# Kernel optimization log

Hardware: AMD Instinct MI355X
Metric: run time of the kernel (lower is better)

The kernel has to match this reference:

```python
import jax, jax.numpy as jnp
import numpy as np

D_MODEL = 1024
D_INNER = 2048
N_EXPERTS = 8
TOP_K = 2
INIT_STD = 0.02


def setup_inputs() -> dict:
    key = jax.random.key(0)
    ks = jax.random.split(key, 6)
    B, S = 2, 2048
    x = jax.random.normal(ks[0], (B, S, D_MODEL), dtype=jnp.float32)
    router_w = jax.random.normal(ks[1], (N_EXPERTS, D_MODEL), dtype=jnp.float32) * (INIT_STD * 0.1)
    router_b = jnp.zeros((N_EXPERTS,), dtype=jnp.float32)
    gate_w = jax.random.normal(ks[2], (N_EXPERTS, D_MODEL, D_INNER), dtype=jnp.float32) * INIT_STD
    up_w = jax.random.normal(ks[3], (N_EXPERTS, D_MODEL, D_INNER), dtype=jnp.float32) * INIT_STD
    down_w = jax.random.normal(ks[4], (N_EXPERTS, D_INNER, D_MODEL), dtype=jnp.float32) * INIT_STD
    return {"x": x, "router_w": router_w, "router_b": router_b,
            "gate_w": gate_w, "up_w": up_w, "down_w": down_w}


def reference(x, router_w, router_b, gate_w, up_w, down_w):
    # Router: softmax over experts, top-k, renormalize top-k probs.
    logits = jnp.einsum('bsd,ed->bse', x, router_w) + router_b          # [B,S,E]
    probs = jax.nn.softmax(logits, axis=-1)
    top_p, top_i = jax.lax.top_k(probs, TOP_K)                           # [B,S,K]
    top_p = top_p / jnp.sum(top_p, axis=-1, keepdims=True)
    # Per-expert combine weight: c[b,s,e] = sum_k top_p[b,s,k] * [top_i[b,s,k]==e]
    onehot = jax.nn.one_hot(top_i, N_EXPERTS, dtype=x.dtype)             # [B,S,K,E]
    combine = jnp.einsum('bsk,bske->bse', top_p, onehot)                 # [B,S,E]
    # SwiGLU FFN for every expert (dense form of the masked dispatch),
    # zeroed/weighted by combine coefficients.
    g = jnp.einsum('bsd,edf->ebsf', x, gate_w)                           # [E,B,S,F]
    u = jnp.einsum('bsd,edf->ebsf', x, up_w)
    h = jax.nn.silu(g) * u
    y = jnp.einsum('ebsf,efd->ebsd', h, down_w)                          # [E,B,S,D]
    out = jnp.einsum('ebsd,bse->bsd', y, combine)
    return out
```

## Files before the change

kernel.cpp:

```cpp
#include <hip/hip_runtime.h>
#include <hip/hip_bf16.h>
#include <stdint.h>

#define D_MODEL 1024
#define D_INNER 2048
#define NEXP 8
#define TOPK 2
#define T256 40
#define T128 72

typedef float f32x4 __attribute__((ext_vector_type(4)));
typedef short bf16x8 __attribute__((ext_vector_type(8)));

#define MEMFENCE asm volatile("" ::: "memory")

__device__ __forceinline__ unsigned short f2b(float f) {
    union { float f; uint32_t u; } v; v.f = f;
    uint32_t u = v.u;
    return (unsigned short)((u + 0x7fffu + ((u >> 16) & 1u)) >> 16);
}

__device__ __forceinline__ void gl_lds16(const void* g, void* l) {
    __builtin_amdgcn_global_load_lds((const __attribute__((address_space(1))) void*)g,
                                     (__attribute__((address_space(3))) void*)l, 16, 0, 0);
}

__global__ __launch_bounds__(256) void tcast3_kernel(
    const float* __restrict__ gw, const float* __restrict__ uw, const float* __restrict__ dw,
    unsigned short* __restrict__ gT, unsigned short* __restrict__ uT, unsigned short* __restrict__ dT)
{
    __shared__ unsigned short S[64][68];
    int which = blockIdx.z >> 3;
    int e = blockIdx.z & 7;
    const float* in; unsigned short* out; int K, N;
    if (which == 0)      { in = gw; out = gT; K = D_MODEL; N = D_INNER; }
    else if (which == 1) { in = uw; out = uT; K = D_MODEL; N = D_INNER; }
    else                 { in = dw; out = dT; K = D_INNER; N = D_MODEL; }
    int n0 = blockIdx.x * 64, k0 = blockIdx.y * 64;
    if (n0 >= N || k0 >= K) return;
    const float* ib = in + (size_t)e * K * N;
    unsigned short* ob = out + (size_t)e * N * K;
    int tid = threadIdx.x;
    int kk = tid >> 4, nn4 = (tid & 15) * 4;
#pragma unroll
    for (int j = 0; j < 4; j++) {
        int k = kk + 16 * j;
        float4 v = *(const float4*)&ib[(size_t)(k0 + k) * N + n0 + nn4];
        ushort4 s; s.x = f2b(v.x); s.y = f2b(v.y); s.z = f2b(v.z); s.w = f2b(v.w);
        *(ushort4*)&S[k][nn4] = s;
    }
    __syncthreads();
    int nn = tid >> 4, kk4 = (tid & 15) * 4;
#pragma unroll
    for (int j = 0; j < 4; j++) {
        int n = nn + 16 * j;
        ushort4 s;
        s.x = S[kk4 + 0][n]; s.y = S[kk4 + 1][n];
        s.z = S[kk4 + 2][n]; s.w = S[kk4 + 3][n];
        *(ushort4*)&ob[(size_t)(n0 + n) * K + k0 + kk4] = s;
    }
}

__global__ __launch_bounds__(64) void router_kernel(
    const float* __restrict__ x, const float* __restrict__ rw,
    const float* __restrict__ rb, unsigned short* __restrict__ xb,
    int* __restrict__ top_i, float* __restrict__ top_w, int T)
{
    int t = blockIdx.x;
    if (t >= T) return;
    int l = threadIdx.x;
    float xv[16];
#pragma unroll
    for (int i = 0; i < 16; i++) xv[i] = x[(size_t)t * D_MODEL + l + 64 * i];
#pragma unroll
    for (int i = 0; i < 16; i++) xb[(size_t)t * D_MODEL + l + 64 * i] = f2b(xv[i]);
    float logit[NEXP];
#pragma unroll
    for (int e = 0; e < NEXP; e++) {
        float acc = 0.f;
#pragma unroll
        for (int i = 0; i < 16; i++) acc += xv[i] * rw[e * D_MODEL + l + 64 * i];
#pragma unroll
        for (int s = 32; s > 0; s >>= 1) acc += __shfl_xor(acc, s, 64);
        logit[e] = acc + rb[e];
    }
    if (l == 0) {
        int i0 = 0; float m0 = logit[0];
#pragma unroll
        for (int e = 1; e < NEXP; e++) if (logit[e] > m0) { m0 = logit[e]; i0 = e; }
        int i1 = -1; float m1 = -3.0e38f;
#pragma unroll
        for (int e = 0; e < NEXP; e++) {
            if (e == i0) continue;
            if (logit[e] > m1) { m1 = logit[e]; i1 = e; }
        }
        float w0 = 1.f / (1.f + expf(m1 - m0));
        top_i[t * 2 + 0] = i0; top_i[t * 2 + 1] = i1;
        top_w[t * 2 + 0] = w0; top_w[t * 2 + 1] = 1.f - w0;
    }
}

__global__ __launch_bounds__(256) void bucket_kernel(
    const int* __restrict__ top_i, const float* __restrict__ top_w,
    int* __restrict__ meta, int* __restrict__ tok_of_slot,
    float* __restrict__ w_of_slot, int T)
{
    __shared__ int cnt[256][NEXP];
    __shared__ int pre[256][NEXP];
    __shared__ int tot[NEXP];
    __shared__ int off[NEXP + 1];
    int tid = threadIdx.x;
    int per = (T + 255) / 256;
    int t0 = tid * per;
    for (int e = 0; e < NEXP; e++) cnt[tid][e] = 0;
    for (int t = t0; t < t0 + per && t < T; t++)
        for (int k = 0; k < TOPK; k++) cnt[tid][top_i[t * 2 + k]]++;
    __syncthreads();
    if (tid < NEXP) {
        int run = 0;
        for (int i = 0; i < 256; i++) { pre[i][tid] = run; run += cnt[i][tid]; }
        tot[tid] = run;
    }
    __syncthreads();
    if (tid == 0) {
        off[0] = 0;
        for (int e = 0; e < NEXP; e++) off[e + 1] = off[e] + tot[e];
        for (int e = 0; e <= NEXP; e++) meta[e] = off[e];
        int nt = 0;
        for (int e = 0; e < NEXP; e++)
            for (int r = off[e]; r < off[e + 1]; r += 256)
                meta[16 + nt++] = (e << 16) | r;
        for (; nt < T256; nt++) meta[16 + nt] = -1;
        nt = 0;
        for (int e = 0; e < NEXP; e++)
            for (int r = off[e]; r < off[e + 1]; r += 128)
                meta[64 + nt++] = (e << 16) | r;
        for (; nt < T128; nt++) meta[64 + nt] = -1;
    }
    __syncthreads();
    int lc[NEXP];
#pragma unroll
    for (int e = 0; e < NEXP; e++) lc[e] = 0;
    for (int t = t0; t < t0 + per && t < T; t++) {
        for (int k = 0; k < TOPK; k++) {
            int e = top_i[t * 2 + k];
            int slot = off[e] + pre[tid][e] + lc[e]++;
            tok_of_slot[slot] = t;
            w_of_slot[slot] = top_w[t * 2 + k];
        }
    }
}

__global__ __launch_bounds__(512, 2) void moe_gate_up(
    const unsigned short* __restrict__ xb, const unsigned short* __restrict__ wgT,
    const unsigned short* __restrict__ wuT, const int* __restrict__ meta,
    const int* __restrict__ tok_of_slot, unsigned short* __restrict__ H)
{
    extern __shared__ __align__(16) unsigned short lds[];

    int lin = blockIdx.x;
    int strip = (lin & 7) * 2 + ((lin >> 3) & 1);
    int tix = lin >> 4;
    int packed = meta[16 + tix];
    if (packed < 0) return;
    int e = packed >> 16, row0 = packed & 0xffff;
    int Mloc = min(256, meta[e + 1] - row0);
    int f0 = strip * 128;

    int tid = threadIdx.x, wv = tid >> 6, lane = tid & 63;
    int c = tid & 7, rr = tid >> 3;

    const unsigned short* srcA[4];
    const unsigned short* srcG[2];
    const unsigned short* srcU[2];
#pragma unroll
    for (int j = 0; j < 4; j++) {
        int row = j * 64 + rr;
        int slot = row0 + ((row < Mloc) ? row : 0);
        srcA[j] = xb + (size_t)tok_of_slot[slot] * D_MODEL + 8 * (c ^ (row & 7));
    }
#pragma unroll
    for (int j = 0; j < 2; j++) {
        int row = j * 64 + rr;
        size_t wb = (size_t)e * D_MODEL * D_INNER + (size_t)(f0 + row) * D_MODEL + 8 * (c ^ (row & 7));
        srcG[j] = wgT + wb; srcU[j] = wuT + wb;
    }

    int wm = wv >> 1, wn = wv & 1;
    int lrow = lane & 15, kgrp = lane >> 4;
    int sw = lrow & 7;
    int co0 = 8 * (kgrp ^ sw);
    int co1 = 8 * ((4 + kgrp) ^ sw);

    int arow[4], brow[4];
#pragma unroll
    for (int i = 0; i < 4; i++) arow[i] = (wm * 64 + i * 16 + lrow) * 64;
#pragma unroll
    for (int i = 0; i < 4; i++) brow[i] = (wn * 64 + i * 16 + lrow) * 64;

    f32x4 accg[4][4], accu[4][4];
#pragma unroll
    for (int i = 0; i < 4; i++)
#pragma unroll
        for (int j = 0; j < 4; j++) {
            accg[i][j] = (f32x4){0.f, 0.f, 0.f, 0.f};
            accu[i][j] = (f32x4){0.f, 0.f, 0.f, 0.f};
        }

    auto stage = [&](int u) {
        int kk = u * 64;
        unsigned short* base = lds + (u & 1) * 32768;
#pragma unroll
        for (int j = 0; j < 4; j++)
            gl_lds16(srcA[j] + kk, base + (j * 512 + wv * 64) * 8);
#pragma unroll
        for (int j = 0; j < 2; j++) {
            gl_lds16(srcG[j] + kk, base + 16384 + (j * 512 + wv * 64) * 8);
            gl_lds16(srcU[j] + kk, base + 24576 + (j * 512 + wv * 64) * 8);
        }
    };

    bf16x8 a[4], bg[4], bu[4];
    auto load_frags = [&](int u, int co) {
        const unsigned short* base = lds + (u & 1) * 32768;
#pragma unroll
        for (int i = 0; i < 4; i++) a[i] = *(const bf16x8*)(base + arow[i] + co);
#pragma unroll
        for (int i = 0; i < 4; i++) bg[i] = *(const bf16x8*)(base + 16384 + brow[i] + co);
#pragma unroll
        for (int i = 0; i < 4; i++) bu[i] = *(const bf16x8*)(base + 24576 + brow[i] + co);
    };

    const int NT = D_MODEL / 64;
    stage(0);
    MEMFENCE;
    asm volatile("s_waitcnt vmcnt(0)" ::: "memory");
    __builtin_amdgcn_s_barrier();
    MEMFENCE;
    load_frags(0, co0);

    for (int t = 0; t < NT; ++t) {
        if (t + 1 < NT) stage(t + 1);
        __builtin_amdgcn_sched_barrier(0);
        __builtin_amdgcn_s_setprio(1);
#pragma unroll
        for (int fm = 0; fm < 4; fm++)
#pragma unroll
            for (int fn = 0; fn < 4; fn++) {
                accg[fm][fn] = __builtin_amdgcn_mfma_f32_16x16x32_bf16(a[fm], bg[fn], accg[fm][fn], 0, 0, 0);
                accu[fm][fn] = __builtin_amdgcn_mfma_f32_16x16x32_bf16(a[fm], bu[fn], accu[fm][fn], 0, 0, 0);
            }
        __builtin_amdgcn_s_setprio(0);
        load_frags(t, co1);
        __builtin_amdgcn_s_setprio(1);
#pragma unroll
        for (int fm = 0; fm < 4; fm++)
#pragma unroll
            for (int fn = 0; fn < 4; fn++) {
                accg[fm][fn] = __builtin_amdgcn_mfma_f32_16x16x32_bf16(a[fm], bg[fn], accg[fm][fn], 0, 0, 0);
                accu[fm][fn] = __builtin_amdgcn_mfma_f32_16x16x32_bf16(a[fm], bu[fn], accu[fm][fn], 0, 0, 0);
            }
        __builtin_amdgcn_s_setprio(0);
        __builtin_amdgcn_sched_barrier(0);
        asm volatile("s_waitcnt vmcnt(0)" ::: "memory");
        __builtin_amdgcn_s_barrier();
        MEMFENCE;
        if (t + 1 < NT) load_frags(t + 1, co0);
    }

#pragma unroll
    for (int fm = 0; fm < 4; fm++)
#pragma unroll
        for (int fn = 0; fn < 4; fn++)
#pragma unroll
            for (int r = 0; r < 4; r++) {
                int m = wm * 64 + fm * 16 + kgrp * 4 + r;
                if (m < Mloc) {
                    int n = wn * 64 + fn * 16 + lrow;
                    float g = accg[fm][fn][r], u = accu[fm][fn][r];
                    float h = g / (1.f + __expf(-g)) * u;
                    H[(size_t)(row0 + m) * D_INNER + f0 + n] = f2b(h);
                }
            }
}

__global__ __launch_bounds__(512, 2) void moe_down(
    const unsigned short* __restrict__ H, const unsigned short* __restrict__ wdT,
    const int* __restrict__ meta, const int* __restrict__ tok_of_slot,
    const float* __restrict__ w_of_slot, float* __restrict__ out, int S2)
{
    extern __shared__ __align__(16) unsigned short lds[];
    __shared__ int toks[128];
    __shared__ float wts[128];

    int lin = blockIdx.x;
    int d0 = (lin & 3) * 256;
    int tix = lin >> 2;
    int packed = meta[64 + tix];
    if (packed < 0) return;
    int e = packed >> 16, row0 = packed & 0xffff;
    int Mloc = min(128, meta[e + 1] - row0);

    int tid = threadIdx.x, wv = tid >> 6, lane = tid & 63;
    if (tid < 128) {
        bool v = tid < Mloc;
        toks[tid] = v ? tok_of_slot[row0 + tid] : 0;
        wts[tid] = v ? w_of_slot[row0 + tid] : 0.f;
    }
    int c = tid & 7, rr = tid >> 3;

    const unsigned short* srcA[2];
    const unsigned short* srcB[4];
#pragma unroll
    for (int j = 0; j < 2; j++) {
        int row = j * 64 + rr;
        int slot = min(row0 + row, S2 - 1);
        srcA[j] = H + (size_t)slot * D_INNER + 8 * (c ^ (row & 7));
    }
#pragma unroll
    for (int j = 0; j < 4; j++) {
        int row = j * 64 + rr;
        srcB[j] = wdT + (size_t)e * D_INNER * D_MODEL + (size_t)(d0 + row) * D_INNER + 8 * (c ^ (row & 7));
    }

    int wm = wv >> 2, wn = wv & 3;
    int lrow = lane & 15, kgrp = lane >> 4;
    int sw = lrow & 7;
    int co0 = 8 * (kgrp ^ sw);
    int co1 = 8 * ((4 + kgrp) ^ sw);

    int arow[4], brow[4];
#pragma unroll
    for (int i = 0; i < 4; i++) arow[i] = (wm * 64 + i * 16 + lrow) * 64;
#pragma unroll
    for (int i = 0; i < 4; i++) brow[i] = 8192 + (wn * 64 + i * 16 + lrow) * 64;

    f32x4 acc[4][4];
#pragma unroll
    for (int i = 0; i < 4; i++)
#pragma unroll
        for (int j = 0; j < 4; j++) acc[i][j] = (f32x4){0.f, 0.f, 0.f, 0.f};

    auto stage = [&](int u) {
        int kk = u * 64;
        unsigned short* base = lds + (u & 1) * 24576;
#pragma unroll
        for (int j = 0; j < 2; j++)
            gl_lds16(srcA[j] + kk, base + (j * 512 + wv * 64) * 8);
#pragma unroll
        for (int j = 0; j < 4; j++)
            gl_lds16(srcB[j] + kk, base + 8192 + (j * 512 + wv * 64) * 8);
    };

    bf16x8 a[4], b[4];
    auto load_frags = [&](int u, int co) {
        const unsigned short* base = lds + (u & 1) * 24576;
#pragma unroll
        for (int i = 0; i < 4; i++) a[i] = *(const bf16x8*)(base + arow[i] + co);
#pragma unroll
        for (int i = 0; i < 4; i++) b[i] = *(const bf16x8*)(base + brow[i] + co);
    };

    const int NT = D_INNER / 64;
    stage(0);
    MEMFENCE;
    asm volatile("s_waitcnt vmcnt(0)" ::: "memory");
    __builtin_amdgcn_s_barrier();
    MEMFENCE;
    load_frags(0, co0);

    for (int t = 0; t < NT; ++t) {
        if (t + 1 < NT) stage(t + 1);
        __builtin_amdgcn_sched_barrier(0);
        __builtin_amdgcn_s_setprio(1);
#pragma unroll
        for (int fm = 0; fm < 4; fm++)
#pragma unroll
            for (int fn = 0; fn < 4; fn++)
                acc[fm][fn] = __builtin_amdgcn_mfma_f32_16x16x32_bf16(a[fm], b[fn], acc[fm][fn], 0, 0, 0);
        __builtin_amdgcn_s_setprio(0);
        load_frags(t, co1);
        __builtin_amdgcn_s_setprio(1);
#pragma unroll
        for (int fm = 0; fm < 4; fm++)
#pragma unroll
            for (int fn = 0; fn < 4; fn++)
                acc[fm][fn] = __builtin_amdgcn_mfma_f32_16x16x32_bf16(a[fm], b[fn], acc[fm][fn], 0, 0, 0);
        __builtin_amdgcn_s_setprio(0);
        __builtin_amdgcn_sched_barrier(0);
        asm volatile("s_waitcnt vmcnt(0)" ::: "memory");
        __builtin_amdgcn_s_barrier();
        MEMFENCE;
        if (t + 1 < NT) load_frags(t + 1, co0);
    }

#pragma unroll
    for (int fm = 0; fm < 4; fm++)
#pragma unroll
        for (int fn = 0; fn < 4; fn++)
#pragma unroll
            for (int r = 0; r < 4; r++) {
                int m = wm * 64 + fm * 16 + kgrp * 4 + r;
                if (m < Mloc) {
                    int n = wn * 64 + fn * 16 + lrow;
                    atomicAdd(&out[(size_t)toks[m] * D_MODEL + d0 + n], wts[m] * acc[fm][fn][r]);
                }
            }
}

extern "C" void kernel_launch(void* const* d_in, const int* in_sizes, int n_in,
                              void* d_out, int out_size, void* d_ws, size_t ws_size,
                              hipStream_t stream) {
    const float* x  = (const float*)d_in[0];
    const float* rw = (const float*)d_in[1];
    const float* rb = (const float*)d_in[2];
    const float* gw = (const float*)d_in[3];
    const float* uw = (const float*)d_in[4];
    const float* dw = (const float*)d_in[5];
    float* out = (float*)d_out;

    int T = in_sizes[0] / D_MODEL;
    int S2 = 2 * T;

    char* ws = (char*)d_ws;
    size_t cur = 0;
    auto take = [&](size_t bytes) { char* p = ws + cur; cur = (cur + bytes + 255) & ~(size_t)255; return p; };
    int*   top_i = (int*)take((size_t)S2 * 4);
    float* top_w = (float*)take((size_t)S2 * 4);
    int*   meta  = (int*)take(1024);
    int*   tos   = (int*)take((size_t)S2 * 4);
    float* wos   = (float*)take((size_t)S2 * 4);
    unsigned short* xb  = (unsigned short*)take((size_t)T * D_MODEL * 2);
    unsigned short* wgT = (unsigned short*)take((size_t)NEXP * D_MODEL * D_INNER * 2);
    unsigned short* wuT = (unsigned short*)take((size_t)NEXP * D_MODEL * D_INNER * 2);
    unsigned short* wdT = (unsigned short*)take((size_t)NEXP * D_MODEL * D_INNER * 2);
    unsigned short* H   = (unsigned short*)take((size_t)S2 * D_INNER * 2);

    static const int GU_LDS = 2 * 32768 * 2;
    static const int DN_LDS = 2 * 24576 * 2;
    hipFuncSetAttribute((const void*)moe_gate_up,
                        hipFuncAttributeMaxDynamicSharedMemorySize, GU_LDS);
    hipFuncSetAttribute((const void*)moe_down,
                        hipFuncAttributeMaxDynamicSharedMemorySize, DN_LDS);

    hipMemsetAsync(d_out, 0, (size_t)out_size * sizeof(float), stream);

    tcast3_kernel<<<dim3(32, 32, 24), 256, 0, stream>>>(gw, uw, dw, wgT, wuT, wdT);
    router_kernel<<<T, 64, 0, stream>>>(x, rw, rb, xb, top_i, top_w, T);
    bucket_kernel<<<1, 256, 0, stream>>>(top_i, top_w, meta, tos, wos, T);

    moe_gate_up<<<T256 * 16, 512, GU_LDS, stream>>>(xb, wgT, wuT, meta, tos, H);
    moe_down<<<T128 * 4, 512, DN_LDS, stream>>>(H, wdT, meta, tos, wos, out, S2);
}
```

Before: 269.8 us.

## Restructure MoE GEMMs into 256-thread 128-row tiles with 3-stage LDS ring

Both expert GEMM kernels move from 512-thread blocks with a double-buffered BK=64 pipeline to 256-thread blocks with BK=32 and a three-slot LDS ring that prefetches two stages ahead using partial vmcnt waits. Gate/up now uses 128-row tiles instead of 256-row tiles. The down projection gains split-K over four quarters of D_INNER, with each wave computing 64x128 outputs. The intent is more blocks and occupancy, better overlap of global loads with MFMA, and less padding waste on ragged expert tiles. The cost is more atomic adds on the output from split-K, re-reading weights across more row tiles in gate/up, and a larger accumulator register footprint in the down kernel.

```diff
diff --git a/kernel.cpp b/kernel.cpp
--- a/kernel.cpp
+++ b/kernel.cpp
@@ -13,6 +13,7 @@
 typedef short bf16x8 __attribute__((ext_vector_type(8)));
 
 #define MEMFENCE asm volatile("" ::: "memory")
+#define SROW(r) ((((r) & 3) ^ (((r) >> 2) & 1)) & 3)
 
 __device__ __forceinline__ unsigned short f2b(float f) {
     union { float f; uint32_t u; } v; v.f = f;
@@ -151,7 +152,51 @@
     }
 }
 
-__global__ __launch_bounds__(512, 2) void moe_gate_up(
+#define GU_MFMA(ACC_, A_, B_)                                                    \
+  _Pragma("unroll") for (int fm_ = 0; fm_ < 4; fm_++)                            \
+    _Pragma("unroll") for (int fn_ = 0; fn_ < 4; fn_++)                          \
+      ACC_[fm_][fn_] = __builtin_amdgcn_mfma_f32_16x16x32_bf16(A_[fm_], B_[fn_], ACC_[fm_][fn_], 0, 0, 0);
+
+#define GU_LOAD_ABG(U_, A_, BG_)                                                 \
+  { const unsigned short* b_ = lds + ((U_) % 3) * 12288;                         \
+    _Pragma("unroll") for (int i_ = 0; i_ < 4; i_++) {                           \
+      A_[i_]  = *(const bf16x8*)(b_ + aoff[i_]);                                 \
+      BG_[i_] = *(const bf16x8*)(b_ + bgoff[i_]);                                \
+    } }
+
+#define GU_LOAD_BU(U_)                                                           \
+  { const unsigned short* b_ = lds + ((U_) % 3) * 12288;                         \
+    _Pragma("unroll") for (int i_ = 0; i_ < 4; i_++)                             \
+      bu[i_] = *(const bf16x8*)(b_ + buoff[i_]);                                 \
+  }
+
+#define GU_ITER(T_, AC_, BGC_, AN_, BGN_)                                        \
+  {                                                                              \
+    int t_ = (T_);                                                               \
+    if (t_ + 2 < 32) stage(t_ + 2);                                              \
+    GU_LOAD_BU(t_);                                                              \
+    __builtin_amdgcn_sched_barrier(0);                                           \
+    __builtin_amdgcn_s_setprio(1);                                               \
+    GU_MFMA(accg, AC_, BGC_);                                                    \
+    __builtin_amdgcn_s_setprio(0);                                               \
+    __builtin_amdgcn_sched_barrier(0);                                           \
+    asm volatile("s_waitcnt lgkmcnt(0)" ::: "memory");                           \
+    __builtin_amdgcn_sched_barrier(0);                                           \
+    if (t_ + 2 < 32) { asm volatile("s_waitcnt vmcnt(6)" ::: "memory"); }        \
+    else             { asm volatile("s_waitcnt vmcnt(0)" ::: "memory"); }        \
+    __builtin_amdgcn_s_barrier();                                                \
+    MEMFENCE;                                                                    \
+    if (t_ + 1 < 32) GU_LOAD_ABG(t_ + 1, AN_, BGN_);                             \
+    __builtin_amdgcn_sched_barrier(0);                                           \
+    __builtin_amdgcn_s_setprio(1);                                               \
+    GU_MFMA(accu, AC_, bu);                                                      \
+    __builtin_amdgcn_s_setprio(0);                                               \
+    __builtin_amdgcn_sched_barrier(0);                                           \
+    asm volatile("s_waitcnt lgkmcnt(0)" ::: "memory");                           \
+    __builtin_amdgcn_sched_barrier(0);                                           \
+  }
+
+__global__ __launch_bounds__(256, 2) void moe_gate_up(
     const unsigned short* __restrict__ xb, const unsigned short* __restrict__ wgT,
     const unsigned short* __restrict__ wuT, const int* __restrict__ meta,
     const int* __restrict__ tok_of_slot, unsigned short* __restrict__ H)
@@ -159,44 +204,47 @@
     extern __shared__ __align__(16) unsigned short lds[];
 
     int lin = blockIdx.x;
-    int strip = (lin & 7) * 2 + ((lin >> 3) & 1);
-    int tix = lin >> 4;
-    int packed = meta[16 + tix];
+    int strip = lin & 15, tix = lin >> 4;
+    int packed = meta[64 + tix];
     if (packed < 0) return;
     int e = packed >> 16, row0 = packed & 0xffff;
-    int Mloc = min(256, meta[e + 1] - row0);
+    int Mloc = min(128, meta[e + 1] - row0);
     int f0 = strip * 128;
 
     int tid = threadIdx.x, wv = tid >> 6, lane = tid & 63;
-    int c = tid & 7, rr = tid >> 3;
-
-    const unsigned short* srcA[4];
-    const unsigned short* srcG[2];
-    const unsigned short* srcU[2];
-#pragma unroll
-    for (int j = 0; j < 4; j++) {
-        int row = j * 64 + rr;
-        int slot = row0 + ((row < Mloc) ? row : 0);
-        srcA[j] = xb + (size_t)tok_of_slot[slot] * D_MODEL + 8 * (c ^ (row & 7));
-    }
-#pragma unroll
-    for (int j = 0; j < 2; j++) {
-        int row = j * 64 + rr;
-        size_t wb = (size_t)e * D_MODEL * D_INNER + (size_t)(f0 + row) * D_MODEL + 8 * (c ^ (row & 7));
-        srcG[j] = wgT + wb; srcU[j] = wuT + wb;
-    }
-
-    int wm = wv >> 1, wn = wv & 1;
+
+    const unsigned short *sA0, *sA1, *sG0, *sG1, *sU0, *sU1;
+    int dA0, dA1;
+    {
+        int c = lane & 3;
+        int q0 = wv * 64 + lane, q1 = 256 + wv * 64 + lane;
+        int r0 = q0 >> 2, r1 = q1 >> 2;
+        int sl0 = row0 + ((r0 < Mloc) ? r0 : 0);
+        int sl1 = row0 + ((r1 < Mloc) ? r1 : 0);
+        sA0 = xb + (size_t)tok_of_slot[sl0] * D_MODEL + (c ^ SROW(r0)) * 8;
+        sA1 = xb + (size_t)tok_of_slot[sl1] * D_MODEL + (c ^ SROW(r1)) * 8;
+        size_t wb0 = (size_t)e * D_MODEL * D_INNER + (size_t)(f0 + r0) * D_MODEL + (c ^ SROW(r0)) * 8;
+        size_t wb1 = (size_t)e * D_MODEL * D_INNER + (size_t)(f0 + r1) * D_MODEL + (c ^ SROW(r1)) * 8;
+        sG0 = wgT + wb0; sG1 = wgT + wb1;
+        sU0 = wuT + wb0; sU1 = wuT + wb1;
+        dA0 = (wv * 64) * 8; dA1 = (256 + wv * 64) * 8;
+    }
+
+    int wm = (wv >> 1) & 1, wn = wv & 1;
     int lrow = lane & 15, kgrp = lane >> 4;
-    int sw = lrow & 7;
-    int co0 = 8 * (kgrp ^ sw);
-    int co1 = 8 * ((4 + kgrp) ^ sw);
-
-    int arow[4], brow[4];
-#pragma unroll
-    for (int i = 0; i < 4; i++) arow[i] = (wm * 64 + i * 16 + lrow) * 64;
-#pragma unroll
-    for (int i = 0; i < 4; i++) brow[i] = (wn * 64 + i * 16 + lrow) * 64;
+    int aoff[4], bgoff[4], buoff[4];
+#pragma unroll
+    for (int i = 0; i < 4; i++) {
+        int r = wm * 64 + i * 16 + lrow;
+        aoff[i] = r * 32 + ((kgrp ^ SROW(r)) & 3) * 8;
+    }
+#pragma unroll
+    for (int i = 0; i < 4; i++) {
+        int r = wn * 64 + i * 16 + lrow;
+        int o = r * 32 + ((kgrp ^ SROW(r)) & 3) * 8;
+        bgoff[i] = 4096 + o;
+        buoff[i] = 8192 + o;
+    }
 
     f32x4 accg[4][4], accu[4][4];
 #pragma unroll
@@ -208,64 +256,30 @@
         }
 
     auto stage = [&](int u) {
-        int kk = u * 64;
-        unsigned short* base = lds + (u & 1) * 32768;
-#pragma unroll
-        for (int j = 0; j < 4; j++)
-            gl_lds16(srcA[j] + kk, base + (j * 512 + wv * 64) * 8);
-#pragma unroll
-        for (int j = 0; j < 2; j++) {
-            gl_lds16(srcG[j] + kk, base + 16384 + (j * 512 + wv * 64) * 8);
-            gl_lds16(srcU[j] + kk, base + 24576 + (j * 512 + wv * 64) * 8);
-        }
+        int kk = u * 32;
+        unsigned short* b = lds + (u % 3) * 12288;
+        gl_lds16(sA0 + kk, b + dA0);
+        gl_lds16(sA1 + kk, b + dA1);
+        gl_lds16(sG0 + kk, b + 4096 + dA0);
+        gl_lds16(sG1 + kk, b + 4096 + dA1);
+        gl_lds16(sU0 + kk, b + 8192 + dA0);
+        gl_lds16(sU1 + kk, b + 8192 + dA1);
     };
 
-    bf16x8 a[4], bg[4], bu[4];
-    auto load_frags = [&](int u, int co) {
-        const unsigned short* base = lds + (u & 1) * 32768;
-#pragma unroll
-        for (int i = 0; i < 4; i++) a[i] = *(const bf16x8*)(base + arow[i] + co);
-#pragma unroll
-        for (int i = 0; i < 4; i++) bg[i] = *(const bf16x8*)(base + 16384 + brow[i] + co);
-#pragma unroll
-        for (int i = 0; i < 4; i++) bu[i] = *(const bf16x8*)(base + 24576 + brow[i] + co);
-    };
-
-    const int NT = D_MODEL / 64;
-    stage(0);
+    bf16x8 aA[4], bgA[4], aB[4], bgB[4], bu[4];
+
+    stage(0); stage(1);
     MEMFENCE;
-    asm volatile("s_waitcnt vmcnt(0)" ::: "memory");
+    asm volatile("s_waitcnt vmcnt(6)" ::: "memory");
     __builtin_amdgcn_s_barrier();
     MEMFENCE;
-    load_frags(0, co0);
-
-    for (int t = 0; t < NT; ++t) {
-        if (t + 1 < NT) stage(t + 1);
-        __builtin_amdgcn_sched_barrier(0);
-        __builtin_amdgcn_s_setprio(1);
-#pragma unroll
-        for (int fm = 0; fm < 4; fm++)
-#pragma unroll
-            for (int fn = 0; fn < 4; fn++) {
-                accg[fm][fn] = __builtin_amdgcn_mfma_f32_16x16x32_bf16(a[fm], bg[fn], accg[fm][fn], 0, 0, 0);
-                accu[fm][fn] = __builtin_amdgcn_mfma_f32_16x16x32_bf16(a[fm], bu[fn], accu[fm][fn], 0, 0, 0);
-            }
-        __builtin_amdgcn_s_setprio(0);
-        load_frags(t, co1);
-        __builtin_amdgcn_s_setprio(1);
-#pragma unroll
-        for (int fm = 0; fm < 4; fm++)
-#pragma unroll
-            for (int fn = 0; fn < 4; fn++) {
-                accg[fm][fn] = __builtin_amdgcn_mfma_f32_16x16x32_bf16(a[fm], bg[fn], accg[fm][fn], 0, 0, 0);
-                accu[fm][fn] = __builtin_amdgcn_mfma_f32_16x16x32_bf16(a[fm], bu[fn], accu[fm][fn], 0, 0, 0);
-            }
-        __builtin_amdgcn_s_setprio(0);
-        __builtin_amdgcn_sched_barrier(0);
-        asm volatile("s_waitcnt vmcnt(0)" ::: "memory");
-        __builtin_amdgcn_s_barrier();
-        MEMFENCE;
-        if (t + 1 < NT) load_frags(t + 1, co0);
+    GU_LOAD_ABG(0, aA, bgA);
+    asm volatile("s_waitcnt lgkmcnt(0)" ::: "memory");
+    __builtin_amdgcn_sched_barrier(0);
+
+    for (int t = 0; t < 32; t += 2) {
+        GU_ITER(t,     aA, bgA, aB, bgB);
+        GU_ITER(t + 1, aB, bgB, aA, bgA);
     }
 
 #pragma unroll
@@ -284,10 +298,55 @@
             }
 }
 
-__global__ __launch_bounds__(512, 2) void moe_down(
+#define DN_MFMA(FNBASE_, A_, B_)                                                 \
+  _Pragma("unroll") for (int fm_ = 0; fm_ < 4; fm_++)                            \
+    _Pragma("unroll") for (int fn_ = 0; fn_ < 4; fn_++)                          \
+      acc[fm_][(FNBASE_) + fn_] = __builtin_amdgcn_mfma_f32_16x16x32_bf16(       \
+          A_[fm_], B_[fn_], acc[fm_][(FNBASE_) + fn_], 0, 0, 0);
+
+#define DN_LOAD_ABLO(U_, A_, BL_)                                                \
+  { const unsigned short* b_ = lds + ((U_) % 3) * 12288;                         \
+    _Pragma("unroll") for (int i_ = 0; i_ < 4; i_++) {                           \
+      A_[i_]  = *(const bf16x8*)(b_ + aoff[i_]);                                 \
+      BL_[i_] = *(const bf16x8*)(b_ + boff[i_]);                                 \
+    } }
+
+#define DN_LOAD_BHI(U_)                                                          \
+  { const unsigned short* b_ = lds + ((U_) % 3) * 12288;                         \
+    _Pragma("unroll") for (int i_ = 0; i_ < 4; i_++)                             \
+      bHi[i_] = *(const bf16x8*)(b_ + boff[4 + i_]);                             \
+  }
+
+#define DN_ITER(T_, AC_, BLC_, AN_, BLN_)                                        \
+  {                                                                              \
+    int t_ = (T_);                                                               \
+    if (t_ + 2 < 16) stage(t_ + 2);                                              \
+    DN_LOAD_BHI(t_);                                                             \
+    __builtin_amdgcn_sched_barrier(0);                                           \
+    __builtin_amdgcn_s_setprio(1);                                               \
+    DN_MFMA(0, AC_, BLC_);                                                       \
+    __builtin_amdgcn_s_setprio(0);                                               \
+    __builtin_amdgcn_sched_barrier(0);                                           \
+    asm volatile("s_waitcnt lgkmcnt(0)" ::: "memory");                           \
+    __builtin_amdgcn_sched_barrier(0);                                           \
+    if (t_ + 2 < 16) { asm volatile("s_waitcnt vmcnt(6)" ::: "memory"); }        \
+    else             { asm volatile("s_waitcnt vmcnt(0)" ::: "memory"); }        \
+    __builtin_amdgcn_s_barrier();                                                \
+    MEMFENCE;                                                                    \
+    if (t_ + 1 < 16) DN_LOAD_ABLO(t_ + 1, AN_, BLN_);                            \
+    __builtin_amdgcn_sched_barrier(0);                                           \
+    __builtin_amdgcn_s_setprio(1);                                               \
+    DN_MFMA(4, AC_, bHi);                                                        \
+    __builtin_amdgcn_s_setprio(0);                                               \
+    __builtin_amdgcn_sched_barrier(0);                                           \
+    asm volatile("s_waitcnt lgkmcnt(0)" ::: "memory");                           \
+    __builtin_amdgcn_sched_barrier(0);                                           \
+  }
+
+__global__ __launch_bounds__(256, 2) void moe_down(
     const unsigned short* __restrict__ H, const unsigned short* __restrict__ wdT,
     const int* __restrict__ meta, const int* __restrict__ tok_of_slot,
-    const float* __restrict__ w_of_slot, float* __restrict__ out, int S2)
+    const float* __restrict__ w_of_slot, float* __restrict__ out)
 {
     extern __shared__ __align__(16) unsigned short lds[];
     __shared__ int toks[128];
@@ -295,11 +354,13 @@
 
     int lin = blockIdx.x;
     int d0 = (lin & 3) * 256;
-    int tix = lin >> 2;
+    int kq = (lin >> 2) & 3;
+    int tix = lin >> 4;
     int packed = meta[64 + tix];
     if (packed < 0) return;
     int e = packed >> 16, row0 = packed & 0xffff;
     int Mloc = min(128, meta[e + 1] - row0);
+    int kb = kq * 512;
 
     int tid = threadIdx.x, wv = tid >> 6, lane = tid & 63;
     if (tid < 128) {
@@ -307,103 +368,90 @@
         toks[tid] = v ? tok_of_slot[row0 + tid] : 0;
         wts[tid] = v ? w_of_slot[row0 + tid] : 0.f;
     }
-    int c = tid & 7, rr = tid >> 3;
-
-    const unsigned short* srcA[2];
-    const unsigned short* srcB[4];
-#pragma unroll
-    for (int j = 0; j < 2; j++) {
-        int row = j * 64 + rr;
-        int slot = min(row0 + row, S2 - 1);
-        srcA[j] = H + (size_t)slot * D_INNER + 8 * (c ^ (row & 7));
-    }
-#pragma unroll
-    for (int j = 0; j < 4; j++) {
-        int row = j * 64 + rr;
-        srcB[j] = wdT + (size_t)e * D_INNER * D_MODEL + (size_t)(d0 + row) * D_INNER + 8 * (c ^ (row & 7));
-    }
-
-    int wm = wv >> 2, wn = wv & 3;
+    __syncthreads();
+
+    const unsigned short *sA0, *sA1, *sB0, *sB1, *sB2, *sB3;
+    int dA0, dA1, dB0, dB1, dB2, dB3;
+    {
+        int c = lane & 3;
+        int qa0 = wv * 64 + lane, qa1 = 256 + wv * 64 + lane;
+        int ra0 = qa0 >> 2, ra1 = qa1 >> 2;
+        int sl0 = row0 + ((ra0 < Mloc) ? ra0 : 0);
+        int sl1 = row0 + ((ra1 < Mloc) ? ra1 : 0);
+        sA0 = H + (size_t)sl0 * D_INNER + kb + (c ^ SROW(ra0)) * 8;
+        sA1 = H + (size_t)sl1 * D_INNER + kb + (c ^ SROW(ra1)) * 8;
+        dA0 = (wv * 64) * 8; dA1 = (256 + wv * 64) * 8;
+        const unsigned short* wbase = wdT + (size_t)e * D_INNER * D_MODEL + kb;
+#pragma unroll
+        for (int j = 0; j < 4; j++) {
+            int q = j * 256 + wv * 64 + lane;
+            int r = q >> 2;
+            const unsigned short* s = wbase + (size_t)(d0 + r) * D_INNER + (c ^ SROW(r)) * 8;
+            int d = 4096 + (j * 256 + wv * 64) * 8;
+            if (j == 0) { sB0 = s; dB0 = d; }
+            else if (j == 1) { sB1 = s; dB1 = d; }
+            else if (j == 2) { sB2 = s; dB2 = d; }
+            else { sB3 = s; dB3 = d; }
+        }
+    }
+
+    int wm = (wv >> 1) & 1, wn = wv & 1;
     int lrow = lane & 15, kgrp = lane >> 4;
-    int sw = lrow & 7;
-    int co0 = 8 * (kgrp ^ sw);
-    int co1 = 8 * ((4 + kgrp) ^ sw);
-
-    int arow[4], brow[4];
-#pragma unroll
-    for (int i = 0; i < 4; i++) arow[i] = (wm * 64 + i * 16 + lrow) * 64;
-#pragma unroll
-    for (int i = 0; i < 4; i++) brow[i] = 8192 + (wn * 64 + i * 16 + lrow) * 64;
-
-    f32x4 acc[4][4];
+    int aoff[4], boff[8];
+#pragma unroll
+    for (int i = 0; i < 4; i++) {
+        int r = wm * 64 + i * 16 + lrow;
+        aoff[i] = r * 32 + ((kgrp ^ SROW(r)) & 3) * 8;
+    }
+#pragma unroll
+    for (int i = 0; i < 8; i++) {
+        int r = wn * 128 + i * 16 + lrow;
+        boff[i] = 4096 + r * 32 + ((kgrp ^ SROW(r)) & 3) * 8;
+    }
+
+    f32x4 acc[4][8];
 #pragma unroll
     for (int i = 0; i < 4; i++)
 #pragma unroll
-        for (int j = 0; j < 4; j++) acc[i][j] = (f32x4){0.f, 0.f, 0.f, 0.f};
+        for (int j = 0; j < 8; j++) acc[i][j] = (f32x4){0.f, 0.f, 0.f, 0.f};
 
     auto stage = [&](int u) {
-        int kk = u * 64;
-        unsigned short* base = lds + (u & 1) * 24576;
-#pragma unroll
-        for (int j = 0; j < 2; j++)
-            gl_lds16(srcA[j] + kk, base + (j * 512 + wv * 64) * 8);
-#pragma unroll
-        for (int j = 0; j < 4; j++)
-            gl_lds16(srcB[j] + kk, base + 8192 + (j * 512 + wv * 64) * 8);
+        int kk = u * 32;
+        unsigned short* b = lds + (u % 3) * 12288;
+        gl_lds16(sA0 + kk, b + dA0);
+        gl_lds16(sA1 + kk, b + dA1);
+        gl_lds16(sB0 + kk, b + dB0);
+        gl_lds16(sB1 + kk, b + dB1);
+        gl_lds16(sB2 + kk, b + dB2);
+        gl_lds16(sB3 + kk, b + dB3);
     };
 
-    bf16x8 a[4], b[4];
-    auto load_frags = [&](int u, int co) {
-        const unsigned short* base = lds + (u & 1) * 24576;
-#pragma unroll
-        for (int i = 0; i < 4; i++) a[i] = *(const bf16x8*)(base + arow[i] + co);
-#pragma unroll
-        for (int i = 0; i < 4; i++) b[i] = *(const bf16x8*)(base + brow[i] + co);
-    };
-
-    const int NT = D_INNER / 64;
-    stage(0);
+    bf16x8 aA[4], bLoA[4], aB[4], bLoB[4], bHi[4];
+
+    stage(0); stage(1);
     MEMFENCE;
-    asm volatile("s_waitcnt vmcnt(0)" ::: "memory");
+    asm volatile("s_waitcnt vmcnt(6)" ::: "memory");
     __builtin_amdgcn_s_barrier();
     MEMFENCE;
-    load_frags(0, co0);
-
-    for (int t = 0; t < NT; ++t) {
-        if (t + 1 < NT) stage(t + 1);
-        __builtin_amdgcn_sched_barrier(0);
-        __builtin_amdgcn_s_setprio(1);
-#pragma unroll
-        for (int fm = 0; fm < 4; fm++)
-#pragma unroll
-            for (int fn = 0; fn < 4; fn++)
-                acc[fm][fn] = __builtin_amdgcn_mfma_f32_16x16x32_bf16(a[fm], b[fn], acc[fm][fn], 0, 0, 0);
-        __builtin_amdgcn_s_setprio(0);
-        load_frags(t, co1);
-        __builtin_amdgcn_s_setprio(1);
-#pragma unroll
-        for (int fm = 0; fm < 4; fm++)
-#pragma unroll
-            for (int fn = 0; fn < 4; fn++)
-                acc[fm][fn] = __builtin_amdgcn_mfma_f32_16x16x32_bf16(a[fm], b[fn], acc[fm][fn], 0, 0, 0);
-        __builtin_amdgcn_s_setprio(0);
-        __builtin_amdgcn_sched_barrier(0);
-        asm volatile("s_waitcnt vmcnt(0)" ::: "memory");
-        __builtin_amdgcn_s_barrier();
-        MEMFENCE;
-        if (t + 1 < NT) load_frags(t + 1, co0);
+    DN_LOAD_ABLO(0, aA, bLoA);
+    asm volatile("s_waitcnt lgkmcnt(0)" ::: "memory");
+    __builtin_amdgcn_sched_barrier(0);
+
+    for (int t = 0; t < 16; t += 2) {
+        DN_ITER(t,     aA, bLoA, aB, bLoB);
+        DN_ITER(t + 1, aB, bLoB, aA, bLoA);
     }
 
 #pragma unroll
     for (int fm = 0; fm < 4; fm++)
 #pragma unroll
-        for (int fn = 0; fn < 4; fn++)
+        for (int fn = 0; fn < 8; fn++)
 #pragma unroll
             for (int r = 0; r < 4; r++) {
                 int m = wm * 64 + fm * 16 + kgrp * 4 + r;
                 if (m < Mloc) {
-                    int n = wn * 64 + fn * 16 + lrow;
-                    atomicAdd(&out[(size_t)toks[m] * D_MODEL + d0 + n], wts[m] * acc[fm][fn][r]);
+                    int n = d0 + wn * 128 + fn * 16 + lrow;
+                    atomicAdd(&out[(size_t)toks[m] * D_MODEL + n], wts[m] * acc[fm][fn][r]);
                 }
             }
 }
@@ -436,12 +484,11 @@
     unsigned short* wdT = (unsigned short*)take((size_t)NEXP * D_MODEL * D_INNER * 2);
     unsigned short* H   = (unsigned short*)take((size_t)S2 * D_INNER * 2);
 
-    static const int GU_LDS = 2 * 32768 * 2;
-    static const int DN_LDS = 2 * 24576 * 2;
+    static const int RING_LDS = 3 * 12288 * 2;
     hipFuncSetAttribute((const void*)moe_gate_up,
-                        hipFuncAttributeMaxDynamicSharedMemorySize, GU_LDS);
+                        hipFuncAttributeMaxDynamicSharedMemorySize, RING_LDS);
     hipFuncSetAttribute((const void*)moe_down,
-                        hipFuncAttributeMaxDynamicSharedMemorySize, DN_LDS);
+                        hipFuncAttributeMaxDynamicSharedMemorySize, RING_LDS);
 
     hipMemsetAsync(d_out, 0, (size_t)out_size * sizeof(float), stream);
 
@@ -449,6 +496,6 @@
     router_kernel<<<T, 64, 0, stream>>>(x, rw, rb, xb, top_i, top_w, T);
     bucket_kernel<<<1, 256, 0, stream>>>(top_i, top_w, meta, tos, wos, T);
 
-    moe_gate_up<<<T256 * 16, 512, GU_LDS, stream>>>(xb, wgT, wuT, meta, tos, H);
-    moe_down<<<T128 * 4, 512, DN_LDS, stream>>>(H, wdT, meta, tos, wos, out, S2);
-}
+    moe_gate_up<<<T128 * 16, 256, RING_LDS, stream>>>(xb, wgT, wuT, meta, tos, H);
+    moe_down<<<T128 * 16, 256, RING_LDS, stream>>>(H, wdT, meta, tos, wos, out);
+}
```

New measurement: 321.6 us. 1.19x slower.

## Use persistent workgroups with atomic work queue for MoE GEMM kernels

Applied to the files above, without the earlier changes.

Both expert GEMM kernels become persistent: 256 workgroups repeatedly pull tile indices from a global atomic counter instead of launching one workgroup per padded tile slot. The bucket kernel now records the real tile counts, so no empty workgroups are launched. Work is also ordered strip-major, so consecutive tiles share the same output strip but use different experts. Launch bounds drop from 2 to 1 waves per SIMD, which lowers occupancy and adds a serialization point on the atomic counter, in exchange for less launch and tail waste.

```diff
diff --git a/kernel.cpp b/kernel.cpp
--- a/kernel.cpp
+++ b/kernel.cpp
@@ -130,11 +130,13 @@
         for (int e = 0; e < NEXP; e++)
             for (int r = off[e]; r < off[e + 1]; r += 256)
                 meta[16 + nt++] = (e << 16) | r;
+        meta[11] = nt;
         for (; nt < T256; nt++) meta[16 + nt] = -1;
         nt = 0;
         for (int e = 0; e < NEXP; e++)
             for (int r = off[e]; r < off[e + 1]; r += 128)
                 meta[64 + nt++] = (e << 16) | r;
+        meta[12] = nt;
         for (; nt < T128; nt++) meta[64 + nt] = -1;
     }
     __syncthreads();
@@ -151,261 +153,277 @@
     }
 }
 
-__global__ __launch_bounds__(512, 2) void moe_gate_up(
+__global__ __launch_bounds__(512, 1) void moe_gate_up(
     const unsigned short* __restrict__ xb, const unsigned short* __restrict__ wgT,
     const unsigned short* __restrict__ wuT, const int* __restrict__ meta,
-    const int* __restrict__ tok_of_slot, unsigned short* __restrict__ H)
+    const int* __restrict__ tok_of_slot, unsigned short* __restrict__ H,
+    int* __restrict__ ctr)
 {
     extern __shared__ __align__(16) unsigned short lds[];
-
-    int lin = blockIdx.x;
-    int strip = (lin & 7) * 2 + ((lin >> 3) & 1);
-    int tix = lin >> 4;
-    int packed = meta[16 + tix];
-    if (packed < 0) return;
-    int e = packed >> 16, row0 = packed & 0xffff;
-    int Mloc = min(256, meta[e + 1] - row0);
-    int f0 = strip * 128;
+    __shared__ int sm_wid;
 
     int tid = threadIdx.x, wv = tid >> 6, lane = tid & 63;
     int c = tid & 7, rr = tid >> 3;
-
-    const unsigned short* srcA[4];
-    const unsigned short* srcG[2];
-    const unsigned short* srcU[2];
-#pragma unroll
-    for (int j = 0; j < 4; j++) {
-        int row = j * 64 + rr;
-        int slot = row0 + ((row < Mloc) ? row : 0);
-        srcA[j] = xb + (size_t)tok_of_slot[slot] * D_MODEL + 8 * (c ^ (row & 7));
-    }
-#pragma unroll
-    for (int j = 0; j < 2; j++) {
-        int row = j * 64 + rr;
-        size_t wb = (size_t)e * D_MODEL * D_INNER + (size_t)(f0 + row) * D_MODEL + 8 * (c ^ (row & 7));
-        srcG[j] = wgT + wb; srcU[j] = wuT + wb;
-    }
-
     int wm = wv >> 1, wn = wv & 1;
     int lrow = lane & 15, kgrp = lane >> 4;
     int sw = lrow & 7;
     int co0 = 8 * (kgrp ^ sw);
     int co1 = 8 * ((4 + kgrp) ^ sw);
-
     int arow[4], brow[4];
 #pragma unroll
     for (int i = 0; i < 4; i++) arow[i] = (wm * 64 + i * 16 + lrow) * 64;
 #pragma unroll
     for (int i = 0; i < 4; i++) brow[i] = (wn * 64 + i * 16 + lrow) * 64;
 
-    f32x4 accg[4][4], accu[4][4];
-#pragma unroll
-    for (int i = 0; i < 4; i++)
+    int n256 = meta[11];
+    int nwork = n256 * 16;
+
+    for (;;) {
+        __syncthreads();
+        if (tid == 0) sm_wid = atomicAdd(ctr, 1);
+        __syncthreads();
+        int wid = sm_wid;
+        if (wid >= nwork) break;
+        int strip = wid / n256, tix = wid - strip * n256;
+        int packed = meta[16 + tix];
+        int e = packed >> 16, row0 = packed & 0xffff;
+        int Mloc = min(256, meta[e + 1] - row0);
+        int f0 = strip * 128;
+
+        const unsigned short* srcA[4];
+        const unsigned short* srcG[2];
+        const unsigned short* srcU[2];
 #pragma unroll
         for (int j = 0; j < 4; j++) {
-            accg[i][j] = (f32x4){0.f, 0.f, 0.f, 0.f};
-            accu[i][j] = (f32x4){0.f, 0.f, 0.f, 0.f};
-        }
-
-    auto stage = [&](int u) {
-        int kk = u * 64;
-        unsigned short* base = lds + (u & 1) * 32768;
-#pragma unroll
-        for (int j = 0; j < 4; j++)
-            gl_lds16(srcA[j] + kk, base + (j * 512 + wv * 64) * 8);
+            int row = j * 64 + rr;
+            int slot = row0 + ((row < Mloc) ? row : 0);
+            srcA[j] = xb + (size_t)tok_of_slot[slot] * D_MODEL + 8 * (c ^ (row & 7));
+        }
 #pragma unroll
         for (int j = 0; j < 2; j++) {
-            gl_lds16(srcG[j] + kk, base + 16384 + (j * 512 + wv * 64) * 8);
-            gl_lds16(srcU[j] + kk, base + 24576 + (j * 512 + wv * 64) * 8);
-        }
-    };
-
-    bf16x8 a[4], bg[4], bu[4];
-    auto load_frags = [&](int u, int co) {
-        const unsigned short* base = lds + (u & 1) * 32768;
-#pragma unroll
-        for (int i = 0; i < 4; i++) a[i] = *(const bf16x8*)(base + arow[i] + co);
-#pragma unroll
-        for (int i = 0; i < 4; i++) bg[i] = *(const bf16x8*)(base + 16384 + brow[i] + co);
-#pragma unroll
-        for (int i = 0; i < 4; i++) bu[i] = *(const bf16x8*)(base + 24576 + brow[i] + co);
-    };
-
-    const int NT = D_MODEL / 64;
-    stage(0);
-    MEMFENCE;
-    asm volatile("s_waitcnt vmcnt(0)" ::: "memory");
-    __builtin_amdgcn_s_barrier();
-    MEMFENCE;
-    load_frags(0, co0);
-
-    for (int t = 0; t < NT; ++t) {
-        if (t + 1 < NT) stage(t + 1);
-        __builtin_amdgcn_sched_barrier(0);
-        __builtin_amdgcn_s_setprio(1);
-#pragma unroll
-        for (int fm = 0; fm < 4; fm++)
-#pragma unroll
-            for (int fn = 0; fn < 4; fn++) {
-                accg[fm][fn] = __builtin_amdgcn_mfma_f32_16x16x32_bf16(a[fm], bg[fn], accg[fm][fn], 0, 0, 0);
-                accu[fm][fn] = __builtin_amdgcn_mfma_f32_16x16x32_bf16(a[fm], bu[fn], accu[fm][fn], 0, 0, 0);
+            int row = j * 64 + rr;
+            size_t wb = (size_t)e * D_MODEL * D_INNER + (size_t)(f0 + row) * D_MODEL + 8 * (c ^ (row & 7));
+            srcG[j] = wgT + wb; srcU[j] = wuT + wb;
+        }
+
+        f32x4 accg[4][4], accu[4][4];
+#pragma unroll
+        for (int i = 0; i < 4; i++)
+#pragma unroll
+            for (int j = 0; j < 4; j++) {
+                accg[i][j] = (f32x4){0.f, 0.f, 0.f, 0.f};
+                accu[i][j] = (f32x4){0.f, 0.f, 0.f, 0.f};
             }
-        __builtin_amdgcn_s_setprio(0);
-        load_frags(t, co1);
-        __builtin_amdgcn_s_setprio(1);
-#pragma unroll
-        for (int fm = 0; fm < 4; fm++)
-#pragma unroll
-            for (int fn = 0; fn < 4; fn++) {
-                accg[fm][fn] = __builtin_amdgcn_mfma_f32_16x16x32_bf16(a[fm], bg[fn], accg[fm][fn], 0, 0, 0);
-                accu[fm][fn] = __builtin_amdgcn_mfma_f32_16x16x32_bf16(a[fm], bu[fn], accu[fm][fn], 0, 0, 0);
+
+        auto stage = [&](int u) {
+            int kk = u * 64;
+            unsigned short* base = lds + (u & 1) * 32768;
+#pragma unroll
+            for (int j = 0; j < 4; j++)
+                gl_lds16(srcA[j] + kk, base + (j * 512 + wv * 64) * 8);
+#pragma unroll
+            for (int j = 0; j < 2; j++) {
+                gl_lds16(srcG[j] + kk, base + 16384 + (j * 512 + wv * 64) * 8);
+                gl_lds16(srcU[j] + kk, base + 24576 + (j * 512 + wv * 64) * 8);
             }
-        __builtin_amdgcn_s_setprio(0);
-        __builtin_amdgcn_sched_barrier(0);
+        };
+
+        bf16x8 a[4], bg[4], bu[4];
+        auto load_frags = [&](int u, int co) {
+            const unsigned short* base = lds + (u & 1) * 32768;
+#pragma unroll
+            for (int i = 0; i < 4; i++) a[i] = *(const bf16x8*)(base + arow[i] + co);
+#pragma unroll
+            for (int i = 0; i < 4; i++) bg[i] = *(const bf16x8*)(base + 16384 + brow[i] + co);
+#pragma unroll
+            for (int i = 0; i < 4; i++) bu[i] = *(const bf16x8*)(base + 24576 + brow[i] + co);
+        };
+
+        const int NT = D_MODEL / 64;
+        stage(0);
+        MEMFENCE;
         asm volatile("s_waitcnt vmcnt(0)" ::: "memory");
         __builtin_amdgcn_s_barrier();
         MEMFENCE;
-        if (t + 1 < NT) load_frags(t + 1, co0);
-    }
-
-#pragma unroll
-    for (int fm = 0; fm < 4; fm++)
-#pragma unroll
-        for (int fn = 0; fn < 4; fn++)
-#pragma unroll
-            for (int r = 0; r < 4; r++) {
-                int m = wm * 64 + fm * 16 + kgrp * 4 + r;
-                if (m < Mloc) {
-                    int n = wn * 64 + fn * 16 + lrow;
-                    float g = accg[fm][fn][r], u = accu[fm][fn][r];
-                    float h = g / (1.f + __expf(-g)) * u;
-                    H[(size_t)(row0 + m) * D_INNER + f0 + n] = f2b(h);
+        load_frags(0, co0);
+
+        for (int t = 0; t < NT; ++t) {
+            if (t + 1 < NT) stage(t + 1);
+            __builtin_amdgcn_sched_barrier(0);
+            __builtin_amdgcn_s_setprio(1);
+#pragma unroll
+            for (int fm = 0; fm < 4; fm++)
+#pragma unroll
+                for (int fn = 0; fn < 4; fn++) {
+                    accg[fm][fn] = __builtin_amdgcn_mfma_f32_16x16x32_bf16(a[fm], bg[fn], accg[fm][fn], 0, 0, 0);
+                    accu[fm][fn] = __builtin_amdgcn_mfma_f32_16x16x32_bf16(a[fm], bu[fn], accu[fm][fn], 0, 0, 0);
                 }
-            }
-}
-
-__global__ __launch_bounds__(512, 2) void moe_down(
+            __builtin_amdgcn_s_setprio(0);
+            load_frags(t, co1);
+            __builtin_amdgcn_s_setprio(1);
+#pragma unroll
+            for (int fm = 0; fm < 4; fm++)
+#pragma unroll
+                for (int fn = 0; fn < 4; fn++) {
+                    accg[fm][fn] = __builtin_amdgcn_mfma_f32_16x16x32_bf16(a[fm], bg[fn], accg[fm][fn], 0, 0, 0);
+                    accu[fm][fn] = __builtin_amdgcn_mfma_f32_16x16x32_bf16(a[fm], bu[fn], accu[fm][fn], 0, 0, 0);
+                }
+            __builtin_amdgcn_s_setprio(0);
+            __builtin_amdgcn_sched_barrier(0);
+            asm volatile("s_waitcnt vmcnt(0)" ::: "memory");
+            __builtin_amdgcn_s_barrier();
+            MEMFENCE;
+            if (t + 1 < NT) load_frags(t + 1, co0);
+        }
+
+#pragma unroll
+        for (int fm = 0; fm < 4; fm++)
+#pragma unroll
+            for (int fn = 0; fn < 4; fn++)
+#pragma unroll
+                for (int r = 0; r < 4; r++) {
+                    int m = wm * 64 + fm * 16 + kgrp * 4 + r;
+                    if (m < Mloc) {
+                        int n = wn * 64 + fn * 16 + lrow;
+                        float g = accg[fm][fn][r], u = accu[fm][fn][r];
+                        float h = g / (1.f + __expf(-g)) * u;
+                        H[(size_t)(row0 + m) * D_INNER + f0 + n] = f2b(h);
+                    }
+                }
+    }
+}
+
+__global__ __launch_bounds__(512, 1) void moe_down(
     const unsigned short* __restrict__ H, const unsigned short* __restrict__ wdT,
     const int* __restrict__ meta, const int* __restrict__ tok_of_slot,
-    const float* __restrict__ w_of_slot, float* __restrict__ out, int S2)
+    const float* __restrict__ w_of_slot, float* __restrict__ out, int S2,
+    int* __restrict__ ctr)
 {
     extern __shared__ __align__(16) unsigned short lds[];
     __shared__ int toks[128];
     __shared__ float wts[128];
-
-    int lin = blockIdx.x;
-    int d0 = (lin & 3) * 256;
-    int tix = lin >> 2;
-    int packed = meta[64 + tix];
-    if (packed < 0) return;
-    int e = packed >> 16, row0 = packed & 0xffff;
-    int Mloc = min(128, meta[e + 1] - row0);
+    __shared__ int sm_wid;
 
     int tid = threadIdx.x, wv = tid >> 6, lane = tid & 63;
-    if (tid < 128) {
-        bool v = tid < Mloc;
-        toks[tid] = v ? tok_of_slot[row0 + tid] : 0;
-        wts[tid] = v ? w_of_slot[row0 + tid] : 0.f;
-    }
     int c = tid & 7, rr = tid >> 3;
-
-    const unsigned short* srcA[2];
-    const unsigned short* srcB[4];
-#pragma unroll
-    for (int j = 0; j < 2; j++) {
-        int row = j * 64 + rr;
-        int slot = min(row0 + row, S2 - 1);
-        srcA[j] = H + (size_t)slot * D_INNER + 8 * (c ^ (row & 7));
-    }
-#pragma unroll
-    for (int j = 0; j < 4; j++) {
-        int row = j * 64 + rr;
-        srcB[j] = wdT + (size_t)e * D_INNER * D_MODEL + (size_t)(d0 + row) * D_INNER + 8 * (c ^ (row & 7));
-    }
-
     int wm = wv >> 2, wn = wv & 3;
     int lrow = lane & 15, kgrp = lane >> 4;
     int sw = lrow & 7;
     int co0 = 8 * (kgrp ^ sw);
     int co1 = 8 * ((4 + kgrp) ^ sw);
-
     int arow[4], brow[4];
 #pragma unroll
     for (int i = 0; i < 4; i++) arow[i] = (wm * 64 + i * 16 + lrow) * 64;
 #pragma unroll
     for (int i = 0; i < 4; i++) brow[i] = 8192 + (wn * 64 + i * 16 + lrow) * 64;
 
-    f32x4 acc[4][4];
-#pragma unroll
-    for (int i = 0; i < 4; i++)
-#pragma unroll
-        for (int j = 0; j < 4; j++) acc[i][j] = (f32x4){0.f, 0.f, 0.f, 0.f};
-
-    auto stage = [&](int u) {
-        int kk = u * 64;
-        unsigned short* base = lds + (u & 1) * 24576;
-#pragma unroll
-        for (int j = 0; j < 2; j++)
-            gl_lds16(srcA[j] + kk, base + (j * 512 + wv * 64) * 8);
-#pragma unroll
-        for (int j = 0; j < 4; j++)
-            gl_lds16(srcB[j] + kk, base + 8192 + (j * 512 + wv * 64) * 8);
-    };
-
-    bf16x8 a[4], b[4];
-    auto load_frags = [&](int u, int co) {
-        const unsigned short* base = lds + (u & 1) * 24576;
-#pragma unroll
-        for (int i = 0; i < 4; i++) a[i] = *(const bf16x8*)(base + arow[i] + co);
-#pragma unroll
-        for (int i = 0; i < 4; i++) b[i] = *(const bf16x8*)(base + brow[i] + co);
-    };
-
-    const int NT = D_INNER / 64;
-    stage(0);
-    MEMFENCE;
-    asm volatile("s_waitcnt vmcnt(0)" ::: "memory");
-    __builtin_amdgcn_s_barrier();
-    MEMFENCE;
-    load_frags(0, co0);
-
-    for (int t = 0; t < NT; ++t) {
-        if (t + 1 < NT) stage(t + 1);
-        __builtin_amdgcn_sched_barrier(0);
-        __builtin_amdgcn_s_setprio(1);
-#pragma unroll
-        for (int fm = 0; fm < 4; fm++)
-#pragma unroll
-            for (int fn = 0; fn < 4; fn++)
-                acc[fm][fn] = __builtin_amdgcn_mfma_f32_16x16x32_bf16(a[fm], b[fn], acc[fm][fn], 0, 0, 0);
-        __builtin_amdgcn_s_setprio(0);
-        load_frags(t, co1);
-        __builtin_amdgcn_s_setprio(1);
-#pragma unroll
-        for (int fm = 0; fm < 4; fm++)
-#pragma unroll
-            for (int fn = 0; fn < 4; fn++)
-                acc[fm][fn] = __builtin_amdgcn_mfma_f32_16x16x32_bf16(a[fm], b[fn], acc[fm][fn], 0, 0, 0);
-        __builtin_amdgcn_s_setprio(0);
-        __builtin_amdgcn_sched_barrier(0);
+    int n128 = meta[12];
+    int nwork = n128 * 4;
+
+    for (;;) {
+        __syncthreads();
+        if (tid == 0) sm_wid = atomicAdd(ctr, 1);
+        __syncthreads();
+        int wid = sm_wid;
+        if (wid >= nwork) break;
+        int dstrip = wid / n128, tix = wid - dstrip * n128;
+        int packed = meta[64 + tix];
+        int e = packed >> 16, row0 = packed & 0xffff;
+        int Mloc = min(128, meta[e + 1] - row0);
+        int d0 = dstrip * 256;
+
+        if (tid < 128) {
+            bool v = tid < Mloc;
+            toks[tid] = v ? tok_of_slot[row0 + tid] : 0;
+            wts[tid] = v ? w_of_slot[row0 + tid] : 0.f;
+        }
+
+        const unsigned short* srcA[2];
+        const unsigned short* srcB[4];
+#pragma unroll
+        for (int j = 0; j < 2; j++) {
+            int row = j * 64 + rr;
+            int slot = min(row0 + row, S2 - 1);
+            srcA[j] = H + (size_t)slot * D_INNER + 8 * (c ^ (row & 7));
+        }
+#pragma unroll
+        for (int j = 0; j < 4; j++) {
+            int row = j * 64 + rr;
+            srcB[j] = wdT + (size_t)e * D_INNER * D_MODEL + (size_t)(d0 + row) * D_INNER + 8 * (c ^ (row & 7));
+        }
+
+        f32x4 acc[4][4];
+#pragma unroll
+        for (int i = 0; i < 4; i++)
+#pragma unroll
+            for (int j = 0; j < 4; j++) acc[i][j] = (f32x4){0.f, 0.f, 0.f, 0.f};
+
+        auto stage = [&](int u) {
+            int kk = u * 64;
+            unsigned short* base = lds + (u & 1) * 24576;
+#pragma unroll
+            for (int j = 0; j < 2; j++)
+                gl_lds16(srcA[j] + kk, base + (j * 512 + wv * 64) * 8);
+#pragma unroll
+            for (int j = 0; j < 4; j++)
+                gl_lds16(srcB[j] + kk, base + 8192 + (j * 512 + wv * 64) * 8);
+        };
+
+        bf16x8 a[4], b[4];
+        auto load_frags = [&](int u, int co) {
+            const unsigned short* base = lds + (u & 1) * 24576;
+#pragma unroll
+            for (int i = 0; i < 4; i++) a[i] = *(const bf16x8*)(base + arow[i] + co);
+#pragma unroll
+            for (int i = 0; i < 4; i++) b[i] = *(const bf16x8*)(base + brow[i] + co);
+        };
+
+        const int NT = D_INNER / 64;
+        stage(0);
+        MEMFENCE;
         asm volatile("s_waitcnt vmcnt(0)" ::: "memory");
         __builtin_amdgcn_s_barrier();
         MEMFENCE;
-        if (t + 1 < NT) load_frags(t + 1, co0);
-    }
-
-#pragma unroll
-    for (int fm = 0; fm < 4; fm++)
-#pragma unroll
-        for (int fn = 0; fn < 4; fn++)
-#pragma unroll
-            for (int r = 0; r < 4; r++) {
-                int m = wm * 64 + fm * 16 + kgrp * 4 + r;
-                if (m < Mloc) {
-                    int n = wn * 64 + fn * 16 + lrow;
-                    atomicAdd(&out[(size_t)toks[m] * D_MODEL + d0 + n], wts[m] * acc[fm][fn][r]);
+        load_frags(0, co0);
+
+        for (int t = 0; t < NT; ++t) {
+            if (t + 1 < NT) stage(t + 1);
+            __builtin_amdgcn_sched_barrier(0);
+            __builtin_amdgcn_s_setprio(1);
+#pragma unroll
+            for (int fm = 0; fm < 4; fm++)
+#pragma unroll
+                for (int fn = 0; fn < 4; fn++)
+                    acc[fm][fn] = __builtin_amdgcn_mfma_f32_16x16x32_bf16(a[fm], b[fn], acc[fm][fn], 0, 0, 0);
+            __builtin_amdgcn_s_setprio(0);
+            load_frags(t, co1);
+            __builtin_amdgcn_s_setprio(1);
+#pragma unroll
+            for (int fm = 0; fm < 4; fm++)
+#pragma unroll
+                for (int fn = 0; fn < 4; fn++)
+                    acc[fm][fn] = __builtin_amdgcn_mfma_f32_16x16x32_bf16(a[fm], b[fn], acc[fm][fn], 0, 0, 0);
+            __builtin_amdgcn_s_setprio(0);
+            __builtin_amdgcn_sched_barrier(0);
+            asm volatile("s_waitcnt vmcnt(0)" ::: "memory");
+            __builtin_amdgcn_s_barrier();
+            MEMFENCE;
+            if (t + 1 < NT) load_frags(t + 1, co0);
+        }
+
+#pragma unroll
+        for (int fm = 0; fm < 4; fm++)
+#pragma unroll
+            for (int fn = 0; fn < 4; fn++)
+#pragma unroll
+                for (int r = 0; r < 4; r++) {
+                    int m = wm * 64 + fm * 16 + kgrp * 4 + r;
+                    if (m < Mloc) {
+                        int n = d0 + wn * 64 + fn * 16 + lrow;
+                        atomicAdd(&out[(size_t)toks[m] * D_MODEL + n], wts[m] * acc[fm][fn][r]);
+                    }
                 }
-            }
+    }
 }
 
 extern "C" void kernel_launch(void* const* d_in, const int* in_sizes, int n_in,
@@ -425,6 +443,7 @@
     char* ws = (char*)d_ws;
     size_t cur = 0;
     auto take = [&](size_t bytes) { char* p = ws + cur; cur = (cur + bytes + 255) & ~(size_t)255; return p; };
+    int*   ctrs  = (int*)take(256);
     int*   top_i = (int*)take((size_t)S2 * 4);
     float* top_w = (float*)take((size_t)S2 * 4);
     int*   meta  = (int*)take(1024);
@@ -443,12 +462,13 @@
     hipFuncSetAttribute((const void*)moe_down,
                         hipFuncAttributeMaxDynamicSharedMemorySize, DN_LDS);
 
+    hipMemsetAsync(ctrs, 0, 256, stream);
     hipMemsetAsync(d_out, 0, (size_t)out_size * sizeof(float), stream);
 
     tcast3_kernel<<<dim3(32, 32, 24), 256, 0, stream>>>(gw, uw, dw, wgT, wuT, wdT);
     router_kernel<<<T, 64, 0, stream>>>(x, rw, rb, xb, top_i, top_w, T);
     bucket_kernel<<<1, 256, 0, stream>>>(top_i, top_w, meta, tos, wos, T);
 
-    moe_gate_up<<<T256 * 16, 512, GU_LDS, stream>>>(xb, wgT, wuT, meta, tos, H);
-    moe_down<<<T128 * 4, 512, DN_LDS, stream>>>(H, wdT, meta, tos, wos, out, S2);
-}
+    moe_gate_up<<<256, 512, GU_LDS, stream>>>(xb, wgT, wuT, meta, tos, H, &ctrs[0]);
+    moe_down<<<256, 512, DN_LDS, stream>>>(H, wdT, meta, tos, wos, out, S2, &ctrs[1]);
+}
```

After: 275.0 us. About the same (+1.9%).
